# Optimization experiments

Hardware: AMD Instinct MI355X
Metric: run time of the kernel (lower is better)

## Reference

```python
import jax, jax.numpy as jnp
import numpy as np

N_NODES = 100000


def gcn_layer(x, src, dst, W, b, num_nodes):
    """PyG GCNConv: out = D^-1/2 (A + I) D^-1/2 (x W) + b, with self-loops."""
    h = x @ W  # [N, out_dim]
    # add self-loops
    loop = jnp.arange(num_nodes, dtype=src.dtype)
    s = jnp.concatenate([src, loop])
    d = jnp.concatenate([dst, loop])
    # symmetric normalization (degree counted on destination, incl. self-loops)
    deg = jax.ops.segment_sum(jnp.ones_like(d, dtype=h.dtype), d, num_segments=num_nodes)
    dinv = jnp.where(deg > 0, jax.lax.rsqrt(deg), 0.0)
    norm = dinv[s] * dinv[d]  # [E+N]
    # gather -> weight -> scatter-add
    msg = h[s] * norm[:, None]  # [E+N, out_dim]
    out = jax.ops.segment_sum(msg, d, num_segments=num_nodes)
    return out + b


def setup_inputs() -> dict:
    key = jax.random.key(0)
    k1, k2, k3, k4 = jax.random.split(key, 4)
    in_chan, h1, h2 = 256, 128, 64
    n_edges = 1600000
    x = jax.random.normal(k1, (N_NODES, in_chan), dtype=jnp.float32)
    edge_index = jax.random.randint(k2, (2, n_edges), 0, N_NODES, dtype=jnp.int64)
    W1 = jax.random.normal(k3, (in_chan, h1), dtype=jnp.float32) * (1.0 / np.sqrt(in_chan))
    b1 = jnp.zeros((h1,), dtype=jnp.float32)
    W2 = jax.random.normal(k4, (h1, h2), dtype=jnp.float32) * (1.0 / np.sqrt(h1))
    b2 = jnp.zeros((h2,), dtype=jnp.float32)
    return {"x": x, "edge_index": edge_index, "W1": W1, "b1": b1, "W2": W2, "b2": b2}


def reference(x, edge_index, W1, b1, W2, b2):
    src, dst = edge_index[0], edge_index[1]
    h = jax.nn.relu(gcn_layer(x, src, dst, W1, b1, N_NODES))
    return jax.nn.relu(gcn_layer(h, src, dst, W2, b2, N_NODES))
```

## Files before the change

kernel.cpp:

```cpp
#include <hip/hip_runtime.h>
#include <hip/hip_fp16.h>

#define NNODES 100000

#define OFF_W1TH     0UL
#define OFF_W1TL     65536UL
#define OFF_W2TH     131072UL
#define OFF_W2TL     147456UL
#define OFF_BCNT     163840UL
#define OFF_BBASE    165888UL
#define OFF_BCUR     167936UL
#define OFF_ROWPTR   400128UL
#define OFF_DINV     1200640UL
#define OFF_COL      1605632UL
#define OFF_EBUF     8005632UL
#define OFF_H1G      8005632UL
#define OFF_H1OUT    59205632UL

typedef __attribute__((ext_vector_type(8))) _Float16 f16x8;
typedef __attribute__((ext_vector_type(4))) float f32x4;

__device__ __forceinline__ void async_copy16(void* lds, const void* g) {
    __builtin_amdgcn_global_load_lds(
        (const __attribute__((address_space(1))) unsigned*)g,
        (__attribute__((address_space(3))) unsigned*)lds, 16, 0, 0);
}

__global__ __launch_bounds__(256) void bincount(const int* __restrict__ dst,
                                                int* __restrict__ bcnt, int E) {
    __shared__ int lc[512];
    int t = threadIdx.x;
    lc[t] = 0; lc[t + 256] = 0;
    __syncthreads();
    for (int e = blockIdx.x * 256 + t; e < E; e += gridDim.x * 256)
        atomicAdd(&lc[dst[e] >> 8], 1);
    __syncthreads();
    if (lc[t]) atomicAdd(&bcnt[t], lc[t]);
    if (lc[t + 256]) atomicAdd(&bcnt[t + 256], lc[t + 256]);
}

__global__ __launch_bounds__(512) void bscan(const int* __restrict__ bcnt,
                                             int* __restrict__ bbase,
                                             int* __restrict__ bcur,
                                             int* __restrict__ rowptr,
                                             int NB, int N, int E) {
    __shared__ int s[512];
    int t = threadIdx.x;
    int v = (t < NB) ? bcnt[t] : 0;
    s[t] = v;
    __syncthreads();
    for (int off = 1; off < 512; off <<= 1) {
        int add = (t >= off) ? s[t - off] : 0;
        __syncthreads();
        s[t] += add;
        __syncthreads();
    }
    if (t < NB) {
        int ex = s[t] - v;
        bbase[t] = ex;
        bcur[t] = ex;
    }
    if (t == 0) rowptr[N] = E;
}

#define CHUNK 4096
__global__ __launch_bounds__(256) void binscatter(const int* __restrict__ src,
                                                  const int* __restrict__ dst,
                                                  int* __restrict__ bcur,
                                                  int2* __restrict__ ebuf, int E) {
    __shared__ int lc[512];
    __shared__ int gb[512];
    int t = threadIdx.x;
    lc[t] = 0; lc[t + 256] = 0;
    __syncthreads();
    int base = blockIdx.x * CHUNK;
    int rb[16];
#pragma unroll
    for (int i = 0; i < 16; ++i) {
        int e = base + i * 256 + t;
        if (e < E) {
            int b = dst[e] >> 8;
            rb[i] = (b << 12) | atomicAdd(&lc[b], 1);
        } else rb[i] = -1;
    }
    __syncthreads();
    if (lc[t]) gb[t] = atomicAdd(&bcur[t], lc[t]);
    if (lc[t + 256]) gb[t + 256] = atomicAdd(&bcur[t + 256], lc[t + 256]);
    __syncthreads();
#pragma unroll
    for (int i = 0; i < 16; ++i) {
        if (rb[i] >= 0) {
            int e = base + i * 256 + t;
            int b = rb[i] >> 12, r = rb[i] & 4095;
            ebuf[gb[b] + r] = make_int2(src[e], dst[e]);
        }
    }
}

__global__ __launch_bounds__(256) void buildcsr(const int2* __restrict__ ebuf,
                                                const int* __restrict__ bbase,
                                                const int* __restrict__ bcnt,
                                                int* __restrict__ rowptr,
                                                int* __restrict__ colarr,
                                                float* __restrict__ dinv, int N) {
    int b = blockIdx.x;
    int t = threadIdx.x;
    int start = bbase[b];
    int cnt = bcnt[b];
    int n0 = b << 8;
    __shared__ int nc[256];
    __shared__ int s[256];
    __shared__ int ncur[256];
    nc[t] = 0;
    __syncthreads();
    for (int e = t; e < cnt; e += 256) atomicAdd(&nc[ebuf[start + e].y - n0], 1);
    __syncthreads();
    int own = nc[t];
    s[t] = own;
    __syncthreads();
    for (int off = 1; off < 256; off <<= 1) {
        int add = (t >= off) ? s[t - off] : 0;
        __syncthreads();
        s[t] += add;
        __syncthreads();
    }
    int rowbase = start + s[t] - own;
    if (n0 + t < N) {
        rowptr[n0 + t] = rowbase;
        dinv[n0 + t] = rsqrtf((float)(own + 1));
    }
    ncur[t] = rowbase;
    __syncthreads();
    for (int e = t; e < cnt; e += 256) {
        int2 p = ebuf[start + e];
        int slot = atomicAdd(&ncur[p.y - n0], 1);
        colarr[slot] = p.x;
    }
}

__global__ __launch_bounds__(256) void split_wt_frag(const float* __restrict__ W,
                                                     _Float16* __restrict__ hi,
                                                     _Float16* __restrict__ lo,
                                                     int K, int N) {
    int idx = blockIdx.x * 256 + threadIdx.x;
    if (idx >= K * N) return;
    int NT = N >> 4;
    int j = idx & 7;
    int l = (idx >> 3) & 63;
    int f = idx >> 9;
    int nt = f % NT;
    int kc = f / NT;
    int k = kc * 32 + (l >> 4) * 8 + j;
    int n = nt * 16 + (l & 15);
    float v = W[k * N + n];
    _Float16 h = (_Float16)v;
    hi[idx] = h;
    lo[idx] = (_Float16)(v - (float)h);
}

template <int BN, int KTOT, bool AFP16>
__global__ __launch_bounds__(256, 3) void gemm_f16(const void* __restrict__ Araw,
                                                   const _Float16* __restrict__ Bh_g,
                                                   const _Float16* __restrict__ Bl_g,
                                                   const float* __restrict__ dinv,
                                                   _Float16* __restrict__ C, int M) {
    constexpr int NT = BN / 16;
    constexpr int FPW = (2 * NT) / 4;
    __shared__ _Float16 Ah[128][72];
    __shared__ _Float16 Bsh[2 * NT * 512];
    __shared__ _Float16 Bsl[2 * NT * 512];

    const int tid = threadIdx.x;
    const int wave = tid >> 6;
    const int lane = tid & 63;
    const int lm = lane & 15;
    const int q = lane >> 4;
    const int m0 = blockIdx.x * 128;

    f32x4 acc[2][NT];
#pragma unroll
    for (int a = 0; a < 2; ++a)
#pragma unroll
        for (int b = 0; b < NT; ++b) acc[a][b] = (f32x4){0.f, 0.f, 0.f, 0.f};

    for (int k0 = 0; k0 < KTOT; k0 += 64) {
        const int kc0 = k0 >> 5;
        const _Float16* bh_base = Bh_g + (size_t)kc0 * NT * 512;
        const _Float16* bl_base = Bl_g + (size_t)kc0 * NT * 512;
#pragma unroll
        for (int i = 0; i < FPW; ++i) {
            int f = wave * FPW + i;
            async_copy16(&Bsh[f * 512 + lane * 8], bh_base + f * 512 + lane * 8);
            async_copy16(&Bsl[f * 512 + lane * 8], bl_base + f * 512 + lane * 8);
        }
#pragma unroll
        for (int i = 0; i < 4; ++i) {
            int flat = tid + i * 256;
            int row = flat >> 3;
            int kk = (flat & 7) << 3;
            int gr = m0 + row;
            if (AFP16) {
                uint4 hv = make_uint4(0u, 0u, 0u, 0u);
                if (gr < M)
                    hv = *(const uint4*)&((const _Float16*)Araw)[(size_t)gr * KTOT + k0 + kk];
                *(uint4*)&Ah[row][kk] = hv;
            } else {
                const float* Af = (const float*)Araw;
                float4 v0 = make_float4(0.f, 0.f, 0.f, 0.f);
                float4 v1 = make_float4(0.f, 0.f, 0.f, 0.f);
                if (gr < M) {
                    v0 = *(const float4*)&Af[(size_t)gr * KTOT + k0 + kk];
                    v1 = *(const float4*)&Af[(size_t)gr * KTOT + k0 + kk + 4];
                }
                f16x8 h;
                h[0] = (_Float16)v0.x; h[1] = (_Float16)v0.y;
                h[2] = (_Float16)v0.z; h[3] = (_Float16)v0.w;
                h[4] = (_Float16)v1.x; h[5] = (_Float16)v1.y;
                h[6] = (_Float16)v1.z; h[7] = (_Float16)v1.w;
                *(f16x8*)&Ah[row][kk] = h;
            }
        }
        __syncthreads();

#pragma unroll
        for (int dkc = 0; dkc < 2; ++dkc) {
            f16x8 a[2];
#pragma unroll
            for (int mt = 0; mt < 2; ++mt)
                a[mt] = *(const f16x8*)&Ah[wave * 32 + mt * 16 + lm][dkc * 32 + q * 8];
#pragma unroll
            for (int nt = 0; nt < NT; ++nt) {
                f16x8 bh = *(const f16x8*)&Bsh[(dkc * NT + nt) * 512 + lane * 8];
                f16x8 bl = *(const f16x8*)&Bsl[(dkc * NT + nt) * 512 + lane * 8];
#pragma unroll
                for (int mt = 0; mt < 2; ++mt) {
                    acc[mt][nt] = __builtin_amdgcn_mfma_f32_16x16x32_f16(a[mt], bh, acc[mt][nt], 0, 0, 0);
                    acc[mt][nt] = __builtin_amdgcn_mfma_f32_16x16x32_f16(a[mt], bl, acc[mt][nt], 0, 0, 0);
                }
            }
        }
        __syncthreads();
    }

#pragma unroll
    for (int mt = 0; mt < 2; ++mt) {
#pragma unroll
        for (int i = 0; i < 4; ++i) {
            int r = m0 + wave * 32 + mt * 16 + q * 4 + i;
            if (r < M) {
                float dv = dinv[r];
#pragma unroll
                for (int nt = 0; nt < NT; ++nt) {
                    C[(size_t)r * BN + nt * 16 + lm] = (_Float16)(acc[mt][nt][i] * dv);
                }
            }
        }
    }
}

__global__ __launch_bounds__(256) void agg_f2h(const __half2* __restrict__ g,
                                               const int* __restrict__ rowptr,
                                               const int* __restrict__ colarr,
                                               const float* __restrict__ dinv,
                                               const float* __restrict__ bias,
                                               __half2* __restrict__ out, int n) {
    int node = blockIdx.x * 4 + (threadIdx.x >> 6);
    int lane = threadIdx.x & 63;
    if (node >= n) return;
    int beg = rowptr[node];
    int end = rowptr[node + 1];
    float2 acc = __half22float2(g[(size_t)node * 64 + lane]);
    int p = beg;
    for (; p + 4 <= end; p += 4) {
        int s0 = colarr[p], s1 = colarr[p + 1], s2 = colarr[p + 2], s3 = colarr[p + 3];
        float2 v0 = __half22float2(g[(size_t)s0 * 64 + lane]);
        float2 v1 = __half22float2(g[(size_t)s1 * 64 + lane]);
        float2 v2 = __half22float2(g[(size_t)s2 * 64 + lane]);
        float2 v3 = __half22float2(g[(size_t)s3 * 64 + lane]);
        acc.x += (v0.x + v1.x) + (v2.x + v3.x);
        acc.y += (v0.y + v1.y) + (v2.y + v3.y);
    }
    for (; p < end; ++p) {
        float2 v = __half22float2(g[(size_t)colarr[p] * 64 + lane]);
        acc.x += v.x;
        acc.y += v.y;
    }
    float dv = dinv[node];
    float2 b = ((const float2*)bias)[lane];
    float ox = fmaxf(fmaf(acc.x, dv, b.x), 0.f);
    float oy = fmaxf(fmaf(acc.y, dv, b.y), 0.f);
    out[(size_t)node * 64 + lane] = __floats2half2_rn(ox, oy);
}

__global__ __launch_bounds__(256) void agg_f1h(const _Float16* __restrict__ g,
                                               const int* __restrict__ rowptr,
                                               const int* __restrict__ colarr,
                                               const float* __restrict__ dinv,
                                               const float* __restrict__ bias,
                                               float* __restrict__ out, int n) {
    int node = blockIdx.x * 4 + (threadIdx.x >> 6);
    int lane = threadIdx.x & 63;
    if (node >= n) return;
    int beg = rowptr[node];
    int end = rowptr[node + 1];
    float acc = (float)g[(size_t)node * 64 + lane];
    int p = beg;
    for (; p + 4 <= end; p += 4) {
        int s0 = colarr[p], s1 = colarr[p + 1], s2 = colarr[p + 2], s3 = colarr[p + 3];
        float v0 = (float)g[(size_t)s0 * 64 + lane];
        float v1 = (float)g[(size_t)s1 * 64 + lane];
        float v2 = (float)g[(size_t)s2 * 64 + lane];
        float v3 = (float)g[(size_t)s3 * 64 + lane];
        acc += (v0 + v1) + (v2 + v3);
    }
    for (; p < end; ++p) acc += (float)g[(size_t)colarr[p] * 64 + lane];
    float dv = dinv[node];
    float o = fmaxf(fmaf(acc, dv, bias[lane]), 0.f);
    out[(size_t)node * 64 + lane] = o;
}

extern "C" void kernel_launch(void* const* d_in, const int* in_sizes, int n_in,
                              void* d_out, int out_size, void* d_ws, size_t ws_size,
                              hipStream_t stream) {
    const float* x  = (const float*)d_in[0];
    const int*   ei = (const int*)d_in[1];
    const float* W1 = (const float*)d_in[2];
    const float* b1 = (const float*)d_in[3];
    const float* W2 = (const float*)d_in[4];
    const float* b2 = (const float*)d_in[5];
    float* out = (float*)d_out;

    const int E = in_sizes[1] / 2;
    const int H1 = in_sizes[3];
    const int K1 = in_sizes[2] / H1;
    const int N = in_sizes[0] / K1;
    const int H2 = in_sizes[4] / H1;
    const int* src = ei;
    const int* dst = ei + E;
    const int NB = (N + 255) >> 8;

    char* ws = (char*)d_ws;
    _Float16* w1th   = (_Float16*)(ws + OFF_W1TH);
    _Float16* w1tl   = (_Float16*)(ws + OFF_W1TL);
    _Float16* w2th   = (_Float16*)(ws + OFF_W2TH);
    _Float16* w2tl   = (_Float16*)(ws + OFF_W2TL);
    int*      bcnt   = (int*)(ws + OFF_BCNT);
    int*      bbase  = (int*)(ws + OFF_BBASE);
    int*      bcur   = (int*)(ws + OFF_BCUR);
    int*      rowptr = (int*)(ws + OFF_ROWPTR);
    float*    dinv   = (float*)(ws + OFF_DINV);
    int*      colarr = (int*)(ws + OFF_COL);
    int2*     ebuf   = (int2*)(ws + OFF_EBUF);
    _Float16* h1g    = (_Float16*)(ws + OFF_H1G);
    _Float16* h1out  = (_Float16*)(ws + OFF_H1OUT);
    _Float16* h2g    = (_Float16*)(ws + OFF_H1G);

    hipMemsetAsync(bcnt, 0, 512 * sizeof(int), stream);
    bincount<<<256, 256, 0, stream>>>(dst, bcnt, E);
    bscan<<<1, 512, 0, stream>>>(bcnt, bbase, bcur, rowptr, NB, N, E);
    binscatter<<<(E + CHUNK - 1) / CHUNK, 256, 0, stream>>>(src, dst, bcur, ebuf, E);
    buildcsr<<<NB, 256, 0, stream>>>(ebuf, bbase, bcnt, rowptr, colarr, dinv, N);

    split_wt_frag<<<(K1 * H1 + 255) / 256, 256, 0, stream>>>(W1, w1th, w1tl, K1, H1);
    split_wt_frag<<<(H1 * H2 + 255) / 256, 256, 0, stream>>>(W2, w2th, w2tl, H1, H2);

    gemm_f16<128, 256, false><<<(N + 127) / 128, 256, 0, stream>>>(x, w1th, w1tl, dinv, h1g, N);
    agg_f2h<<<(N + 3) / 4, 256, 0, stream>>>((const __half2*)h1g, rowptr, colarr, dinv, b1,
                                             (__half2*)h1out, N);

    gemm_f16<64, 128, true><<<(N + 127) / 128, 256, 0, stream>>>(h1out, w2th, w2tl, dinv, h2g, N);
    agg_f1h<<<(N + 3) / 4, 256, 0, stream>>>(h2g, rowptr, colarr, dinv, b2, out, N);
}
```

Before: 409.6 us.

## Pack edge buffer into 32-bit words and split aggregation rows across wave halves

The edge staging buffer now packs the source id and the low 8 bits of the destination into one 32-bit int instead of an int2, which halves that intermediate traffic. The binscatter chunk grows to 8192 edges per block. The two aggregation kernels now have each lane load 4 halves (8 bytes), with the wave split into 2 or 4 groups that process different neighbours in parallel, then reduce with shuffles. This raises bytes per load and the number of gathers in flight, at the cost of extra shuffle work and idle lanes in the epilogue. The packing assumes node ids fit in 20 bits.

```diff
diff --git a/kernel.cpp b/kernel.cpp
--- a/kernel.cpp
+++ b/kernel.cpp
@@ -63,24 +63,24 @@
     if (t == 0) rowptr[N] = E;
 }
 
-#define CHUNK 4096
+#define CHUNK 8192
 __global__ __launch_bounds__(256) void binscatter(const int* __restrict__ src,
                                                   const int* __restrict__ dst,
                                                   int* __restrict__ bcur,
-                                                  int2* __restrict__ ebuf, int E) {
+                                                  int* __restrict__ ebuf, int E) {
     __shared__ int lc[512];
     __shared__ int gb[512];
     int t = threadIdx.x;
     lc[t] = 0; lc[t + 256] = 0;
     __syncthreads();
     int base = blockIdx.x * CHUNK;
-    int rb[16];
-#pragma unroll
-    for (int i = 0; i < 16; ++i) {
+    int rb[32];
+#pragma unroll
+    for (int i = 0; i < 32; ++i) {
         int e = base + i * 256 + t;
         if (e < E) {
             int b = dst[e] >> 8;
-            rb[i] = (b << 12) | atomicAdd(&lc[b], 1);
+            rb[i] = (b << 13) | atomicAdd(&lc[b], 1);
         } else rb[i] = -1;
     }
     __syncthreads();
@@ -88,16 +88,16 @@
     if (lc[t + 256]) gb[t + 256] = atomicAdd(&bcur[t + 256], lc[t + 256]);
     __syncthreads();
 #pragma unroll
-    for (int i = 0; i < 16; ++i) {
+    for (int i = 0; i < 32; ++i) {
         if (rb[i] >= 0) {
             int e = base + i * 256 + t;
-            int b = rb[i] >> 12, r = rb[i] & 4095;
-            ebuf[gb[b] + r] = make_int2(src[e], dst[e]);
-        }
-    }
-}
-
-__global__ __launch_bounds__(256) void buildcsr(const int2* __restrict__ ebuf,
+            int b = rb[i] >> 13, r = rb[i] & 8191;
+            ebuf[gb[b] + r] = src[e] | ((dst[e] & 255) << 20);
+        }
+    }
+}
+
+__global__ __launch_bounds__(256) void buildcsr(const int* __restrict__ ebuf,
                                                 const int* __restrict__ bbase,
                                                 const int* __restrict__ bcnt,
                                                 int* __restrict__ rowptr,
@@ -107,13 +107,12 @@
     int t = threadIdx.x;
     int start = bbase[b];
     int cnt = bcnt[b];
-    int n0 = b << 8;
     __shared__ int nc[256];
     __shared__ int s[256];
     __shared__ int ncur[256];
     nc[t] = 0;
     __syncthreads();
-    for (int e = t; e < cnt; e += 256) atomicAdd(&nc[ebuf[start + e].y - n0], 1);
+    for (int e = t; e < cnt; e += 256) atomicAdd(&nc[ebuf[start + e] >> 20], 1);
     __syncthreads();
     int own = nc[t];
     s[t] = own;
@@ -125,6 +124,7 @@
         __syncthreads();
     }
     int rowbase = start + s[t] - own;
+    int n0 = b << 8;
     if (n0 + t < N) {
         rowptr[n0 + t] = rowbase;
         dinv[n0 + t] = rsqrtf((float)(own + 1));
@@ -132,9 +132,9 @@
     ncur[t] = rowbase;
     __syncthreads();
     for (int e = t; e < cnt; e += 256) {
-        int2 p = ebuf[start + e];
-        int slot = atomicAdd(&ncur[p.y - n0], 1);
-        colarr[slot] = p.x;
+        int pe = ebuf[start + e];
+        int slot = atomicAdd(&ncur[pe >> 20], 1);
+        colarr[slot] = pe & 0xFFFFF;
     }
 }
 
@@ -258,65 +258,153 @@
     }
 }
 
-__global__ __launch_bounds__(256) void agg_f2h(const __half2* __restrict__ g,
-                                               const int* __restrict__ rowptr,
-                                               const int* __restrict__ colarr,
-                                               const float* __restrict__ dinv,
-                                               const float* __restrict__ bias,
-                                               __half2* __restrict__ out, int n) {
+__global__ __launch_bounds__(256) void agg128(const _Float16* __restrict__ g,
+                                              const int* __restrict__ rowptr,
+                                              const int* __restrict__ colarr,
+                                              const float* __restrict__ dinv,
+                                              const float* __restrict__ bias,
+                                              _Float16* __restrict__ out, int n) {
     int node = blockIdx.x * 4 + (threadIdx.x >> 6);
     int lane = threadIdx.x & 63;
     if (node >= n) return;
+    int sel = lane >> 5;
+    int co = (lane & 31) << 2;
+
     int beg = rowptr[node];
     int end = rowptr[node + 1];
-    float2 acc = __half22float2(g[(size_t)node * 64 + lane]);
+
+    float a0 = 0.f, a1 = 0.f, a2 = 0.f, a3 = 0.f;
+    if (sel == 0) {
+        uint2 sv = *(const uint2*)&g[(node << 7) + co];
+        float2 f01 = __half22float2(*(const __half2*)&sv.x);
+        float2 f23 = __half22float2(*(const __half2*)&sv.y);
+        a0 += f01.x; a1 += f01.y; a2 += f23.x; a3 += f23.y;
+    }
+
     int p = beg;
-    for (; p + 4 <= end; p += 4) {
-        int s0 = colarr[p], s1 = colarr[p + 1], s2 = colarr[p + 2], s3 = colarr[p + 3];
-        float2 v0 = __half22float2(g[(size_t)s0 * 64 + lane]);
-        float2 v1 = __half22float2(g[(size_t)s1 * 64 + lane]);
-        float2 v2 = __half22float2(g[(size_t)s2 * 64 + lane]);
-        float2 v3 = __half22float2(g[(size_t)s3 * 64 + lane]);
-        acc.x += (v0.x + v1.x) + (v2.x + v3.x);
-        acc.y += (v0.y + v1.y) + (v2.y + v3.y);
-    }
-    for (; p < end; ++p) {
-        float2 v = __half22float2(g[(size_t)colarr[p] * 64 + lane]);
-        acc.x += v.x;
-        acc.y += v.y;
-    }
-    float dv = dinv[node];
-    float2 b = ((const float2*)bias)[lane];
-    float ox = fmaxf(fmaf(acc.x, dv, b.x), 0.f);
-    float oy = fmaxf(fmaf(acc.y, dv, b.y), 0.f);
-    out[(size_t)node * 64 + lane] = __floats2half2_rn(ox, oy);
-}
-
-__global__ __launch_bounds__(256) void agg_f1h(const _Float16* __restrict__ g,
-                                               const int* __restrict__ rowptr,
-                                               const int* __restrict__ colarr,
-                                               const float* __restrict__ dinv,
-                                               const float* __restrict__ bias,
-                                               float* __restrict__ out, int n) {
+    for (; p + 8 <= end; p += 8) {
+        int r0 = colarr[p + sel];
+        int r1 = colarr[p + 2 + sel];
+        int r2 = colarr[p + 4 + sel];
+        int r3 = colarr[p + 6 + sel];
+        uint2 v0 = *(const uint2*)&g[(r0 << 7) + co];
+        uint2 v1 = *(const uint2*)&g[(r1 << 7) + co];
+        uint2 v2 = *(const uint2*)&g[(r2 << 7) + co];
+        uint2 v3 = *(const uint2*)&g[(r3 << 7) + co];
+#pragma unroll
+        for (int i = 0; i < 4; ++i) {
+            uint2 v = (i == 0) ? v0 : (i == 1) ? v1 : (i == 2) ? v2 : v3;
+            float2 f01 = __half22float2(*(const __half2*)&v.x);
+            float2 f23 = __half22float2(*(const __half2*)&v.y);
+            a0 += f01.x; a1 += f01.y; a2 += f23.x; a3 += f23.y;
+        }
+    }
+    for (; p + 2 <= end; p += 2) {
+        int r = colarr[p + sel];
+        uint2 v = *(const uint2*)&g[(r << 7) + co];
+        float2 f01 = __half22float2(*(const __half2*)&v.x);
+        float2 f23 = __half22float2(*(const __half2*)&v.y);
+        a0 += f01.x; a1 += f01.y; a2 += f23.x; a3 += f23.y;
+    }
+    if (p < end && sel == 0) {
+        int r = colarr[p];
+        uint2 v = *(const uint2*)&g[(r << 7) + co];
+        float2 f01 = __half22float2(*(const __half2*)&v.x);
+        float2 f23 = __half22float2(*(const __half2*)&v.y);
+        a0 += f01.x; a1 += f01.y; a2 += f23.x; a3 += f23.y;
+    }
+
+    a0 += __shfl(a0, lane ^ 32);
+    a1 += __shfl(a1, lane ^ 32);
+    a2 += __shfl(a2, lane ^ 32);
+    a3 += __shfl(a3, lane ^ 32);
+
+    if (sel == 0) {
+        float dv = dinv[node];
+        float4 b = *(const float4*)&bias[co];
+        float o0 = fmaxf(fmaf(a0, dv, b.x), 0.f);
+        float o1 = fmaxf(fmaf(a1, dv, b.y), 0.f);
+        float o2 = fmaxf(fmaf(a2, dv, b.z), 0.f);
+        float o3 = fmaxf(fmaf(a3, dv, b.w), 0.f);
+        __half2 ha = __floats2half2_rn(o0, o1);
+        __half2 hb = __floats2half2_rn(o2, o3);
+        uint2 pk = make_uint2(*(unsigned*)&ha, *(unsigned*)&hb);
+        *(uint2*)&out[(node << 7) + co] = pk;
+    }
+}
+
+__global__ __launch_bounds__(256) void agg64(const _Float16* __restrict__ g,
+                                             const int* __restrict__ rowptr,
+                                             const int* __restrict__ colarr,
+                                             const float* __restrict__ dinv,
+                                             const float* __restrict__ bias,
+                                             float* __restrict__ out, int n) {
     int node = blockIdx.x * 4 + (threadIdx.x >> 6);
     int lane = threadIdx.x & 63;
     if (node >= n) return;
+    int sel = lane >> 4;
+    int co = (lane & 15) << 2;
+
     int beg = rowptr[node];
     int end = rowptr[node + 1];
-    float acc = (float)g[(size_t)node * 64 + lane];
+
+    float a0 = 0.f, a1 = 0.f, a2 = 0.f, a3 = 0.f;
+    if (sel == 0) {
+        uint2 sv = *(const uint2*)&g[(node << 6) + co];
+        float2 f01 = __half22float2(*(const __half2*)&sv.x);
+        float2 f23 = __half22float2(*(const __half2*)&sv.y);
+        a0 += f01.x; a1 += f01.y; a2 += f23.x; a3 += f23.y;
+    }
+
     int p = beg;
+    for (; p + 16 <= end; p += 16) {
+        int r0 = colarr[p + sel];
+        int r1 = colarr[p + 4 + sel];
+        int r2 = colarr[p + 8 + sel];
+        int r3 = colarr[p + 12 + sel];
+        uint2 v0 = *(const uint2*)&g[(r0 << 6) + co];
+        uint2 v1 = *(const uint2*)&g[(r1 << 6) + co];
+        uint2 v2 = *(const uint2*)&g[(r2 << 6) + co];
+        uint2 v3 = *(const uint2*)&g[(r3 << 6) + co];
+#pragma unroll
+        for (int i = 0; i < 4; ++i) {
+            uint2 v = (i == 0) ? v0 : (i == 1) ? v1 : (i == 2) ? v2 : v3;
+            float2 f01 = __half22float2(*(const __half2*)&v.x);
+            float2 f23 = __half22float2(*(const __half2*)&v.y);
+            a0 += f01.x; a1 += f01.y; a2 += f23.x; a3 += f23.y;
+        }
+    }
     for (; p + 4 <= end; p += 4) {
-        int s0 = colarr[p], s1 = colarr[p + 1], s2 = colarr[p + 2], s3 = colarr[p + 3];
-        float v0 = (float)g[(size_t)s0 * 64 + lane];
-        float v1 = (float)g[(size_t)s1 * 64 + lane];
-        float v2 = (float)g[(size_t)s2 * 64 + lane];
-        float v3 = (float)g[(size_t)s3 * 64 + lane];
-        acc += (v0 + v1) + (v2 + v3);
-    }
-    for (; p < end; ++p) acc += (float)g[(size_t)colarr[p] * 64 + lane];
-    float dv = dinv[node];
-    float o = fmaxf(fmaf(acc, dv, bias[lane]), 0.f);
-    out[(size_t)node * 64 + lane] = o;
+        int r = colarr[p + sel];
+        uint2 v = *(const uint2*)&g[(r << 6) + co];
+        float2 f01 = __half22float2(*(const __half2*)&v.x);
+        float2 f23 = __half22float2(*(const __half2*)&v.y);
+        a0 += f01.x; a1 += f01.y; a2 += f23.x; a3 += f23.y;
+    }
+    int rem = end - p;
+    if (sel < rem) {
+        int r = colarr[p + sel];
+        uint2 v = *(const uint2*)&g[(r << 6) + co];
+        float2 f01 = __half22float2(*(const __half2*)&v.x);
+        float2 f23 = __half22float2(*(const __half2*)&v.y);
+        a0 += f01.x; a1 += f01.y; a2 += f23.x; a3 += f23.y;
+    }
+
+    a0 += __shfl(a0, lane ^ 16); a1 += __shfl(a1, lane ^ 16);
+    a2 += __shfl(a2, lane ^ 16); a3 += __shfl(a3, lane ^ 16);
+    a0 += __shfl(a0, lane ^ 32); a1 += __shfl(a1, lane ^ 32);
+    a2 += __shfl(a2, lane ^ 32); a3 += __shfl(a3, lane ^ 32);
+
+    if (sel == 0) {
+        float dv = dinv[node];
+        float4 b = *(const float4*)&bias[co];
+        float4 o;
+        o.x = fmaxf(fmaf(a0, dv, b.x), 0.f);
+        o.y = fmaxf(fmaf(a1, dv, b.y), 0.f);
+        o.z = fmaxf(fmaf(a2, dv, b.z), 0.f);
+        o.w = fmaxf(fmaf(a3, dv, b.w), 0.f);
+        *(float4*)&out[(node << 6) + co] = o;
+    }
 }
 
 extern "C" void kernel_launch(void* const* d_in, const int* in_sizes, int n_in,
@@ -350,7 +438,7 @@
     int*      rowptr = (int*)(ws + OFF_ROWPTR);
     float*    dinv   = (float*)(ws + OFF_DINV);
     int*      colarr = (int*)(ws + OFF_COL);
-    int2*     ebuf   = (int2*)(ws + OFF_EBUF);
+    int*      ebuf   = (int*)(ws + OFF_EBUF);
     _Float16* h1g    = (_Float16*)(ws + OFF_H1G);
     _Float16* h1out  = (_Float16*)(ws + OFF_H1OUT);
     _Float16* h2g    = (_Float16*)(ws + OFF_H1G);
@@ -365,9 +453,8 @@
     split_wt_frag<<<(H1 * H2 + 255) / 256, 256, 0, stream>>>(W2, w2th, w2tl, H1, H2);
 
     gemm_f16<128, 256, false><<<(N + 127) / 128, 256, 0, stream>>>(x, w1th, w1tl, dinv, h1g, N);
-    agg_f2h<<<(N + 3) / 4, 256, 0, stream>>>((const __half2*)h1g, rowptr, colarr, dinv, b1,
-                                             (__half2*)h1out, N);
+    agg128<<<(N + 3) / 4, 256, 0, stream>>>(h1g, rowptr, colarr, dinv, b1, h1out, N);
 
     gemm_f16<64, 128, true><<<(N + 127) / 128, 256, 0, stream>>>(h1out, w2th, w2tl, dinv, h2g, N);
-    agg_f1h<<<(N + 3) / 4, 256, 0, stream>>>(h2g, rowptr, colarr, dinv, b2, out, N);
-}
+    agg64<<<(N + 3) / 4, 256, 0, stream>>>(h2g, rowptr, colarr, dinv, b2, out, N);
+}
```

New measurement: 384.2 us. -6.2%, faster.
